# Optimization experiments

Measured on AMD Instinct MI355X. Metric: run time of the kernel, lower is better.

Reference implementation:

```python
import jax, jax.numpy as jnp
import numpy as np

B, N, DIM = 32, 1024, 512
H, KD, ATTN_RATIO = 8, 64, 4
D = ATTN_RATIO * KD            # value dim per head = 256
DH = D * H                     # 2048
QKV_OUT = DH + 2 * H * KD      # 3072
RES = 32                       # resolution (32, 32), N = 32*32
SCALE = KD ** -0.5


def _make_bias_idxs(res):
    coords = np.stack(np.meshgrid(np.arange(res), np.arange(res), indexing="ij"), -1).reshape(-1, 2)  # [N,2]
    off = np.abs(coords[:, None, :] - coords[None, :, :])  # [N,N,2]
    return jnp.asarray(off[..., 0] * res + off[..., 1], dtype=jnp.int32)  # [N,N] in [0, res*res)


def setup_inputs() -> dict:
    key = jax.random.key(0)
    ks = jax.random.split(key, 6)
    x = jax.random.normal(ks[0], (B, N, DIM), dtype=jnp.float32)
    gamma = jnp.ones((DIM,), jnp.float32)
    beta = jnp.zeros((DIM,), jnp.float32)
    qkv_w = jax.random.normal(ks[1], (DIM, QKV_OUT), jnp.float32) * 0.02
    qkv_b = jnp.zeros((QKV_OUT,), jnp.float32)
    proj_w = jax.random.normal(ks[2], (DH, DIM), jnp.float32) * 0.02
    proj_b = jnp.zeros((DIM,), jnp.float32)
    biases = jax.random.normal(ks[3], (H, RES * RES), jnp.float32) * 0.02
    bias_idxs = _make_bias_idxs(RES)
    return {"x": x, "gamma": gamma, "beta": beta, "qkv_w": qkv_w, "qkv_b": qkv_b,
            "proj_w": proj_w, "proj_b": proj_b, "biases": biases, "bias_idxs": bias_idxs}


def reference(x, gamma, beta, qkv_w, qkv_b, proj_w, proj_b, biases, bias_idxs):
    # LayerNorm
    mu = jnp.mean(x, axis=-1, keepdims=True)
    var = jnp.mean(jnp.square(x - mu), axis=-1, keepdims=True)
    xn = (x - mu) * jax.lax.rsqrt(var + 1e-5) * gamma + beta
    # QKV projection and head split
    qkv = (xn @ qkv_w + qkv_b).reshape(B, N, H, 2 * KD + D)
    q, k, v = jnp.split(qkv, [KD, 2 * KD], axis=-1)  # [B,N,H,KD],[B,N,H,KD],[B,N,H,D]
    # Attention with relative-position bias
    bias = biases[:, bias_idxs]  # [H,N,N]
    attn = jnp.einsum("bqhd,bkhd->bhqk", q, k) * SCALE + bias[None]
    attn = jax.nn.softmax(attn, axis=-1)
    out = jnp.einsum("bhqk,bkhd->bqhd", attn, v).reshape(B, N, DH)
    return out @ proj_w + proj_b
```

## Files before the change

### kernel.cpp

```cpp
#include <hip/hip_runtime.h>
#include <hip/hip_bf16.h>
#include <initializer_list>

typedef _Float16 half8 __attribute__((ext_vector_type(8)));
typedef float floatx4 __attribute__((ext_vector_type(4)));

#define MFMA16(a, b, c) __builtin_amdgcn_mfma_f32_16x16x32_f16((a), (b), (c), 0, 0, 0)

__device__ __forceinline__ void gload16(const void* g, void* l) {
    __builtin_amdgcn_global_load_lds((const __attribute__((address_space(1))) unsigned int*)g,
                                     (__attribute__((address_space(3))) unsigned int*)l,
                                     16, 0, 0);
}

__global__ __launch_bounds__(256) void ln_kernel(const float* __restrict__ x,
                                                 const float* __restrict__ gamma,
                                                 const float* __restrict__ beta,
                                                 _Float16* __restrict__ xn) {
    int row = blockIdx.x;
    int tid = threadIdx.x;
    float2 v = ((const float2*)(x + (size_t)row * 512))[tid];

    __shared__ float red[4];
    __shared__ float mv[2];

    float s = v.x + v.y;
#pragma unroll
    for (int o = 32; o > 0; o >>= 1) s += __shfl_down(s, o);
    if ((tid & 63) == 0) red[tid >> 6] = s;
    __syncthreads();
    if (tid == 0) mv[0] = (red[0] + red[1] + red[2] + red[3]) * (1.f / 512.f);
    __syncthreads();
    float mean = mv[0];

    float dx = v.x - mean, dy = v.y - mean;
    float sq = dx * dx + dy * dy;
#pragma unroll
    for (int o = 32; o > 0; o >>= 1) sq += __shfl_xor(sq, o);
    __syncthreads();
    if ((tid & 63) == 0) red[tid >> 6] = sq;
    __syncthreads();
    if (tid == 0) mv[1] = rsqrtf((red[0] + red[1] + red[2] + red[3]) * (1.f / 512.f) + 1e-5f);
    __syncthreads();
    float rstd = mv[1];

    float g0 = gamma[tid * 2], g1 = gamma[tid * 2 + 1];
    float b0 = beta[tid * 2], b1 = beta[tid * 2 + 1];
    union { _Float16 h[2]; unsigned int u; } pk;
    pk.h[0] = (_Float16)(dx * rstd * g0 + b0);
    pk.h[1] = (_Float16)(dy * rstd * g1 + b1);
    ((unsigned int*)(xn + (size_t)row * 512))[tid] = pk.u;
}

__global__ __launch_bounds__(256) void transpose_cast(const float* __restrict__ in,
                                                      _Float16* __restrict__ out,
                                                      int R, int C) {
    __shared__ float t[32][33];
    int c0 = blockIdx.x * 32, r0 = blockIdx.y * 32;
    int tx = threadIdx.x & 31, ty = threadIdx.x >> 5;
#pragma unroll
    for (int j = 0; j < 4; ++j)
        t[ty + j * 8][tx] = in[(size_t)(r0 + ty + j * 8) * C + c0 + tx];
    __syncthreads();
#pragma unroll
    for (int j = 0; j < 4; ++j)
        out[(size_t)(c0 + ty + j * 8) * R + r0 + tx] = (_Float16)t[tx][ty + j * 8];
}

template <int OUTMODE>
__global__ __launch_bounds__(256) void gemm_bt(const _Float16* __restrict__ A,
                                               const _Float16* __restrict__ Bt,
                                               const float* __restrict__ bias,
                                               void* __restrict__ Cout,
                                               _Float16* __restrict__ Vt,
                                               int M, int N, int K) {
    __shared__ __align__(16) _Float16 Asb[128 * 32];
    __shared__ __align__(16) _Float16 Bsb[128 * 32];

    int m0 = blockIdx.x * 128;
    int n0 = blockIdx.y * 128;
    int tid = threadIdx.x;
    int w = tid >> 6, lane = tid & 63, lrow = lane & 15, quad = lane >> 4;
    int wm = (w >> 1) * 64, wn = (w & 1) * 64;

    int hh = 0, part = 0;
    bool sw = false;
    if (OUTMODE == 2) {
        hh = blockIdx.y / 3;
        part = blockIdx.y - hh * 3;
        sw = (part != 0);
    }

    int srow = lane >> 2;
    int scb = (lane & 3) ^ ((lane >> 3) & 3);
    const _Float16* Abase = A + (size_t)(m0 + w * 16 + srow) * K + scb * 8;
    const _Float16* Bbase = Bt + (size_t)(n0 + w * 16 + srow) * K + scb * 8;
    char* AldsB = (char*)Asb + w * 1024;
    char* BldsB = (char*)Bsb + w * 1024;
    const size_t rowskip = (size_t)64 * K;

    int swz = (lrow >> 1) & 3;

    floatx4 acc[4][4];
#pragma unroll
    for (int i = 0; i < 4; ++i)
#pragma unroll
        for (int j = 0; j < 4; ++j) acc[i][j] = (floatx4){0.f, 0.f, 0.f, 0.f};

    for (int k0 = 0; k0 < K; k0 += 32) {
        __syncthreads();
        gload16(Abase + k0, AldsB);
        gload16(Abase + rowskip + k0, AldsB + 4096);
        gload16(Bbase + k0, BldsB);
        gload16(Bbase + rowskip + k0, BldsB + 4096);
        __syncthreads();

        half8 af[4], bf[4];
#pragma unroll
        for (int i = 0; i < 4; ++i) {
            int r = wm + i * 16 + lrow;
            af[i] = *(const half8*)&Asb[r * 32 + (quad ^ swz) * 8];
        }
#pragma unroll
        for (int j = 0; j < 4; ++j) {
            int r = wn + j * 16 + lrow;
            bf[j] = *(const half8*)&Bsb[r * 32 + (quad ^ swz) * 8];
        }
        if (OUTMODE == 2 && sw) {
#pragma unroll
            for (int i = 0; i < 4; ++i)
#pragma unroll
                for (int j = 0; j < 4; ++j)
                    acc[i][j] = MFMA16(bf[j], af[i], acc[i][j]);
        } else {
#pragma unroll
            for (int i = 0; i < 4; ++i)
#pragma unroll
                for (int j = 0; j < 4; ++j)
                    acc[i][j] = MFMA16(af[i], bf[j], acc[i][j]);
        }
    }

    if (OUTMODE == 2 && sw) {
        int b_rel = m0 >> 10;
        int tok0 = (m0 & 1023) + wm;
        _Float16* vbase = Vt + (((size_t)b_rel * 8 + hh) * 256 + (part - 1) * 128) * 1024;
#pragma unroll
        for (int j = 0; j < 4; ++j)
#pragma unroll
            for (int r = 0; r < 4; ++r) {
                int d = wn + j * 16 + quad * 4 + r;
                float bv = bias[n0 + d];
                _Float16* vrow = vbase + (size_t)d * 1024 + tok0;
#pragma unroll
                for (int i = 0; i < 4; ++i)
                    vrow[i * 16 + lrow] = (_Float16)(acc[i][j][r] + bv);
            }
        return;
    }

#pragma unroll
    for (int i = 0; i < 4; ++i)
#pragma unroll
        for (int j = 0; j < 4; ++j) {
            int colg = n0 + wn + j * 16 + lrow;
            int coll = wn + j * 16 + lrow;
            float bv = bias[colg];
#pragma unroll
            for (int r = 0; r < 4; ++r) {
                int rowg = m0 + wm + i * 16 + quad * 4 + r;
                float v = acc[i][j][r] + bv;
                if (OUTMODE == 1) {
                    ((float*)Cout)[(size_t)rowg * N + colg] = v;
                } else {
                    ((_Float16*)Cout)[(size_t)rowg * 1024 + hh * 128 + coll] = (_Float16)v;
                }
            }
        }
}

__global__ __launch_bounds__(256) void attn_kernel(const _Float16* __restrict__ qk,
                                                   const _Float16* __restrict__ vt,
                                                   const float* __restrict__ biases,
                                                   _Float16* __restrict__ out) {
    int h  = blockIdx.x & 7;
    int qt = (blockIdx.x >> 3) | (blockIdx.y << 1);
    int b  = blockIdx.z;

    int tid = threadIdx.x;
    int w = tid >> 6, lane = tid & 63, lrow = lane & 15, quad = lane >> 4;

    __shared__ float bias_lds[1024];
    __shared__ __align__(16) _Float16 K_lds[32 * 72];
    __shared__ __align__(16) _Float16 V_t[256 * 32];

    for (int i = tid; i < 1024; i += 256) bias_lds[i] = biases[h * 1024 + i];

    int qrow = qt * 64 + w * 16 + lrow;
    const _Float16* qbase = qk + ((size_t)(b * 1024 + qrow)) * 1024 + h * 128;
    half8 aq0 = *(const half8*)(qbase + quad * 8);
    half8 aq1 = *(const half8*)(qbase + 32 + quad * 8);

    int key_l = tid >> 3, kd8 = (tid & 7) * 8;
    const _Float16* ksrc = qk + ((size_t)(b * 1024 + key_l)) * 1024 + h * 128 + 64 + kd8;
    int cc = tid & 3;
    const _Float16* vsrc0 = vt + ((size_t)((b * 8 + h) * 256 + (tid >> 2))) * 1024 + cc * 4;

    int qr = qrow >> 5, qc = qrow & 31;
    int bcol0[4], bcol1[4];
#pragma unroll
    for (int r = 0; r < 4; ++r) {
        bcol0[r] = abs(qc - (quad * 4 + r));
        bcol1[r] = abs(qc - (16 + quad * 4 + r));
    }

    float m_r = -1e30f, l_r = 0.f;
    floatx4 od[16];
#pragma unroll
    for (int dt = 0; dt < 16; ++dt) od[dt] = (floatx4){0.f, 0.f, 0.f, 0.f};

    uint4 kreg;
    uint2 vA[4], vB[4];

    kreg = *(const uint4*)ksrc;
#pragma unroll
    for (int it = 0; it < 4; ++it) {
        const _Float16* p = vsrc0 + (size_t)it * 64 * 1024;
        vA[it] = *(const uint2*)p;
        vB[it] = *(const uint2*)(p + 16);
    }

    for (int kt = 0; kt < 32; ++kt) {
        *(uint4*)&K_lds[key_l * 72 + kd8] = kreg;
#pragma unroll
        for (int it = 0; it < 4; ++it) {
            uint4 v;
            v.x = vA[it].x; v.y = vA[it].y; v.z = vB[it].x; v.w = vB[it].y;
            *(uint4*)&V_t[((tid >> 2) + it * 64) * 32 + cc * 8] = v;
        }
        __syncthreads();

        if (kt < 31) {
            kreg = *(const uint4*)(ksrc + (size_t)(kt + 1) * 32 * 1024);
            const _Float16* vp = vsrc0 + (size_t)(kt + 1) * 32;
#pragma unroll
            for (int it = 0; it < 4; ++it) {
                const _Float16* p = vp + (size_t)it * 64 * 1024;
                vA[it] = *(const uint2*)p;
                vB[it] = *(const uint2*)(p + 16);
            }
        }

        floatx4 sc0 = (floatx4){0.f, 0.f, 0.f, 0.f}, sc1 = sc0;
        {
            half8 kf;
            kf = *(const half8*)&K_lds[lrow * 72 + quad * 8];              sc0 = MFMA16(kf, aq0, sc0);
            kf = *(const half8*)&K_lds[lrow * 72 + 32 + quad * 8];         sc0 = MFMA16(kf, aq1, sc0);
            kf = *(const half8*)&K_lds[(16 + lrow) * 72 + quad * 8];       sc1 = MFMA16(kf, aq0, sc1);
            kf = *(const half8*)&K_lds[(16 + lrow) * 72 + 32 + quad * 8];  sc1 = MFMA16(kf, aq1, sc1);
        }

        int rowoff = abs(qr - kt) << 5;
        float s0[4], s1[4];
#pragma unroll
        for (int r = 0; r < 4; ++r) {
            s0[r] = sc0[r] * 0.125f + bias_lds[rowoff + bcol0[r]];
            s1[r] = sc1[r] * 0.125f + bias_lds[rowoff + bcol1[r]];
        }

        float pmax = fmaxf(fmaxf(fmaxf(s0[0], s0[1]), fmaxf(s0[2], s0[3])),
                           fmaxf(fmaxf(s1[0], s1[1]), fmaxf(s1[2], s1[3])));
        pmax = fmaxf(pmax, __shfl_xor(pmax, 16));
        pmax = fmaxf(pmax, __shfl_xor(pmax, 32));

        if (!__all(pmax - m_r <= 8.f)) {
            float mnew = fmaxf(m_r, pmax);
            float alpha = __expf(m_r - mnew);
            m_r = mnew;
            l_r *= alpha;
            float a4[4];
#pragma unroll
            for (int r = 0; r < 4; ++r) a4[r] = __shfl(alpha, quad * 4 + r, 16);
#pragma unroll
            for (int dt = 0; dt < 16; ++dt)
#pragma unroll
                for (int r = 0; r < 4; ++r) od[dt][r] *= a4[r];
        }

        float p0[4], p1[4], rs = 0.f;
#pragma unroll
        for (int r = 0; r < 4; ++r) { p0[r] = __expf(s0[r] - m_r); rs += p0[r]; }
#pragma unroll
        for (int r = 0; r < 4; ++r) { p1[r] = __expf(s1[r] - m_r); rs += p1[r]; }
        rs += __shfl_xor(rs, 16);
        rs += __shfl_xor(rs, 32);
        l_r += rs;

        union H8 { _Float16 h[8]; half8 v; } pa;
#pragma unroll
        for (int r = 0; r < 4; ++r) { pa.h[r] = (_Float16)p0[r]; pa.h[4 + r] = (_Float16)p1[r]; }

#pragma unroll
        for (int dt = 0; dt < 16; ++dt) {
            half8 bv = *(const half8*)&V_t[(dt * 16 + lrow) * 32 + quad * 8];
            od[dt] = MFMA16(pa.v, bv, od[dt]);
        }
        __syncthreads();
    }

#pragma unroll
    for (int r = 0; r < 4; ++r) {
        float lq = __shfl(l_r, quad * 4 + r, 16);
        float inv = 1.f / lq;
        int qg = qt * 64 + w * 16 + quad * 4 + r;
        _Float16* orow = out + ((size_t)(b * 1024 + qg)) * 2048 + h * 256;
#pragma unroll
        for (int dt = 0; dt < 16; ++dt)
            orow[dt * 16 + lrow] = (_Float16)(od[dt][r] * inv);
    }
}

extern "C" void kernel_launch(void* const* d_in, const int* in_sizes, int n_in,
                              void* d_out, int out_size, void* d_ws, size_t ws_size,
                              hipStream_t stream) {
    const float* x      = (const float*)d_in[0];
    const float* gamma  = (const float*)d_in[1];
    const float* beta   = (const float*)d_in[2];
    const float* qkv_w  = (const float*)d_in[3];
    const float* qkv_b  = (const float*)d_in[4];
    const float* proj_w = (const float*)d_in[5];
    const float* proj_b = (const float*)d_in[6];
    const float* biases = (const float*)d_in[7];

    float* out = (float*)d_out;

    _Float16* ws      = (_Float16*)d_ws;
    _Float16* qkv_wt  = ws;
    _Float16* proj_wt = qkv_wt + (size_t)512 * 3072;
    _Float16* xn      = proj_wt + (size_t)2048 * 512;
    _Float16* chunk0  = xn + (size_t)32768 * 512;

    const size_t FIXED_HALVES = (size_t)512 * 3072 + (size_t)2048 * 512 + (size_t)32768 * 512;
    int CB = 0;
    for (int cb : {16, 8, 4, 2, 1}) {
        size_t halves = FIXED_HALVES + (size_t)cb * 1024 * (1024 + 2048 + 2048);
        if (halves * sizeof(_Float16) <= ws_size) { CB = cb; break; }
    }
    if (CB == 0) return;
    _Float16* qk_c  = chunk0;
    _Float16* vt_c  = qk_c + (size_t)CB * 1024 * 1024;
    _Float16* att_c = vt_c + (size_t)CB * 1024 * 2048;

    transpose_cast<<<dim3(3072 / 32, 512 / 32), 256, 0, stream>>>(qkv_w, qkv_wt, 512, 3072);
    transpose_cast<<<dim3(512 / 32, 2048 / 32), 256, 0, stream>>>(proj_w, proj_wt, 2048, 512);
    ln_kernel<<<32768, 256, 0, stream>>>(x, gamma, beta, xn);

    const int MC = CB * 1024;
    for (int c = 0; c < 32 / CB; ++c) {
        const _Float16* xn_c = xn + (size_t)c * MC * 512;
        gemm_bt<2><<<dim3(MC / 128, 24), 256, 0, stream>>>(xn_c, qkv_wt, qkv_b,
                                                           (void*)qk_c, vt_c, MC, 3072, 512);
        attn_kernel<<<dim3(16, 8, CB), 256, 0, stream>>>(qk_c, vt_c, biases, att_c);
        float* out_c = out + (size_t)c * MC * 512;
        gemm_bt<1><<<dim3(MC / 128, 4), 256, 0, stream>>>(att_c, proj_wt, proj_b,
                                                          (void*)out_c, nullptr, MC, 512, 2048);
    }
}
```

Baseline: 791.6 us.

## Double query rows per wave and double-buffer K/V tiles in attention

```diff
diff --git a/kernel.cpp b/kernel.cpp
--- a/kernel.cpp
+++ b/kernel.cpp
@@ -183,141 +183,166 @@
                                                    const _Float16* __restrict__ vt,
                                                    const float* __restrict__ biases,
                                                    _Float16* __restrict__ out) {
-    int h  = blockIdx.x & 7;
-    int qt = (blockIdx.x >> 3) | (blockIdx.y << 1);
+    int h  = blockIdx.x;
+    int qt = blockIdx.y;
     int b  = blockIdx.z;
 
     int tid = threadIdx.x;
     int w = tid >> 6, lane = tid & 63, lrow = lane & 15, quad = lane >> 4;
 
     __shared__ float bias_lds[1024];
-    __shared__ __align__(16) _Float16 K_lds[32 * 72];
-    __shared__ __align__(16) _Float16 V_t[256 * 32];
+    __shared__ __align__(16) _Float16 K_lds[2][32 * 72];
+    __shared__ __align__(16) _Float16 V_s[2][256 * 32];
 
     for (int i = tid; i < 1024; i += 256) bias_lds[i] = biases[h * 1024 + i];
 
-    int qrow = qt * 64 + w * 16 + lrow;
-    const _Float16* qbase = qk + ((size_t)(b * 1024 + qrow)) * 1024 + h * 128;
-    half8 aq0 = *(const half8*)(qbase + quad * 8);
-    half8 aq1 = *(const half8*)(qbase + 32 + quad * 8);
+    int q0 = qt * 128 + w * 32 + lrow;
+    const _Float16* qb = qk + ((size_t)(b * 1024 + q0)) * 1024 + h * 128;
+    half8 aq[2][2];
+    aq[0][0] = *(const half8*)(qb + quad * 8);
+    aq[0][1] = *(const half8*)(qb + 32 + quad * 8);
+    aq[1][0] = *(const half8*)(qb + 16 * 1024 + quad * 8);
+    aq[1][1] = *(const half8*)(qb + 16 * 1024 + 32 + quad * 8);
 
     int key_l = tid >> 3, kd8 = (tid & 7) * 8;
     const _Float16* ksrc = qk + ((size_t)(b * 1024 + key_l)) * 1024 + h * 128 + 64 + kd8;
     int cc = tid & 3;
     const _Float16* vsrc0 = vt + ((size_t)((b * 8 + h) * 256 + (tid >> 2))) * 1024 + cc * 4;
 
-    int qr = qrow >> 5, qc = qrow & 31;
-    int bcol0[4], bcol1[4];
-#pragma unroll
-    for (int r = 0; r < 4; ++r) {
-        bcol0[r] = abs(qc - (quad * 4 + r));
-        bcol1[r] = abs(qc - (16 + quad * 4 + r));
-    }
-
-    float m_r = -1e30f, l_r = 0.f;
-    floatx4 od[16];
-#pragma unroll
-    for (int dt = 0; dt < 16; ++dt) od[dt] = (floatx4){0.f, 0.f, 0.f, 0.f};
+    int qr = qt * 4 + w;
+
+    float m_[2] = {-1e30f, -1e30f}, l_[2] = {0.f, 0.f};
+    floatx4 od[2][16];
+#pragma unroll
+    for (int f = 0; f < 2; ++f)
+#pragma unroll
+        for (int dt = 0; dt < 16; ++dt) od[f][dt] = (floatx4){0.f, 0.f, 0.f, 0.f};
 
     uint4 kreg;
     uint2 vA[4], vB[4];
 
-    kreg = *(const uint4*)ksrc;
-#pragma unroll
-    for (int it = 0; it < 4; ++it) {
-        const _Float16* p = vsrc0 + (size_t)it * 64 * 1024;
-        vA[it] = *(const uint2*)p;
-        vB[it] = *(const uint2*)(p + 16);
-    }
+#define LOADT(t)                                                          \
+    do {                                                                  \
+        kreg = *(const uint4*)(ksrc + (size_t)(t) * 32 * 1024);           \
+        const _Float16* vp = vsrc0 + (size_t)(t) * 32;                    \
+        _Pragma("unroll") for (int it = 0; it < 4; ++it) {                \
+            const _Float16* p = vp + (size_t)it * 64 * 1024;              \
+            vA[it] = *(const uint2*)p;                                    \
+            vB[it] = *(const uint2*)(p + 16);                             \
+        }                                                                 \
+    } while (0)
+
+#define WRITET(bb)                                                        \
+    do {                                                                  \
+        *(uint4*)&K_lds[bb][key_l * 72 + kd8] = kreg;                     \
+        _Pragma("unroll") for (int it = 0; it < 4; ++it) {                \
+            uint4 v;                                                      \
+            v.x = vA[it].x; v.y = vA[it].y; v.z = vB[it].x; v.w = vB[it].y; \
+            *(uint4*)&V_s[bb][((tid >> 2) + it * 64) * 32 + cc * 8] = v;  \
+        }                                                                 \
+    } while (0)
+
+    LOADT(0);
+    WRITET(0);
+    LOADT(1);
+    __syncthreads();
 
     for (int kt = 0; kt < 32; ++kt) {
-        *(uint4*)&K_lds[key_l * 72 + kd8] = kreg;
-#pragma unroll
-        for (int it = 0; it < 4; ++it) {
-            uint4 v;
-            v.x = vA[it].x; v.y = vA[it].y; v.z = vB[it].x; v.w = vB[it].y;
-            *(uint4*)&V_t[((tid >> 2) + it * 64) * 32 + cc * 8] = v;
+        int bufc = kt & 1;
+        const _Float16* Kc = K_lds[bufc];
+        const _Float16* Vc = V_s[bufc];
+
+        floatx4 sc[2][2];
+#pragma unroll
+        for (int f = 0; f < 2; ++f)
+#pragma unroll
+            for (int t = 0; t < 2; ++t) sc[f][t] = (floatx4){0.f, 0.f, 0.f, 0.f};
+        {
+            half8 kf00 = *(const half8*)&Kc[lrow * 72 + quad * 8];
+            half8 kf01 = *(const half8*)&Kc[lrow * 72 + 32 + quad * 8];
+            half8 kf10 = *(const half8*)&Kc[(16 + lrow) * 72 + quad * 8];
+            half8 kf11 = *(const half8*)&Kc[(16 + lrow) * 72 + 32 + quad * 8];
+#pragma unroll
+            for (int f = 0; f < 2; ++f) {
+                sc[f][0] = MFMA16(kf00, aq[f][0], sc[f][0]);
+                sc[f][0] = MFMA16(kf01, aq[f][1], sc[f][0]);
+                sc[f][1] = MFMA16(kf10, aq[f][0], sc[f][1]);
+                sc[f][1] = MFMA16(kf11, aq[f][1], sc[f][1]);
+            }
+        }
+
+        int rowoff = abs(qr - kt) << 5;
+        union H8 { _Float16 hh[8]; half8 v; } pa[2];
+
+#pragma unroll
+        for (int f = 0; f < 2; ++f) {
+            int qcf = lrow + f * 16;
+            float s_[8];
+#pragma unroll
+            for (int t = 0; t < 2; ++t)
+#pragma unroll
+                for (int r = 0; r < 4; ++r) {
+                    int kc = t * 16 + quad * 4 + r;
+                    s_[t * 4 + r] = sc[f][t][r] * 0.125f + bias_lds[rowoff + abs(qcf - kc)];
+                }
+
+            float pmax = fmaxf(fmaxf(fmaxf(s_[0], s_[1]), fmaxf(s_[2], s_[3])),
+                               fmaxf(fmaxf(s_[4], s_[5]), fmaxf(s_[6], s_[7])));
+            pmax = fmaxf(pmax, __shfl_xor(pmax, 16));
+            pmax = fmaxf(pmax, __shfl_xor(pmax, 32));
+
+            if (!__all(pmax - m_[f] <= 8.f)) {
+                float mnew = fmaxf(m_[f], pmax);
+                float alpha = __expf(m_[f] - mnew);
+                m_[f] = mnew;
+                l_[f] *= alpha;
+                float a4[4];
+#pragma unroll
+                for (int r = 0; r < 4; ++r) a4[r] = __shfl(alpha, quad * 4 + r, 16);
+#pragma unroll
+                for (int dt = 0; dt < 16; ++dt)
+#pragma unroll
+                    for (int r = 0; r < 4; ++r) od[f][dt][r] *= a4[r];
+            }
+
+            float rs = 0.f;
+#pragma unroll
+            for (int i = 0; i < 8; ++i) {
+                float p = __expf(s_[i] - m_[f]);
+                pa[f].hh[i] = (_Float16)p;
+                rs += p;
+            }
+            rs += __shfl_xor(rs, 16);
+            rs += __shfl_xor(rs, 32);
+            l_[f] += rs;
+        }
+
+        if (kt < 31) WRITET(bufc ^ 1);
+        if (kt < 30) LOADT(kt + 2);
+
+#pragma unroll
+        for (int dt = 0; dt < 16; ++dt) {
+            half8 bv = *(const half8*)&Vc[(dt * 16 + lrow) * 32 + quad * 8];
+            od[0][dt] = MFMA16(pa[0].v, bv, od[0][dt]);
+            od[1][dt] = MFMA16(pa[1].v, bv, od[1][dt]);
         }
         __syncthreads();
-
-        if (kt < 31) {
-            kreg = *(const uint4*)(ksrc + (size_t)(kt + 1) * 32 * 1024);
-            const _Float16* vp = vsrc0 + (size_t)(kt + 1) * 32;
-#pragma unroll
-            for (int it = 0; it < 4; ++it) {
-                const _Float16* p = vp + (size_t)it * 64 * 1024;
-                vA[it] = *(const uint2*)p;
-                vB[it] = *(const uint2*)(p + 16);
-            }
-        }
-
-        floatx4 sc0 = (floatx4){0.f, 0.f, 0.f, 0.f}, sc1 = sc0;
-        {
-            half8 kf;
-            kf = *(const half8*)&K_lds[lrow * 72 + quad * 8];              sc0 = MFMA16(kf, aq0, sc0);
-            kf = *(const half8*)&K_lds[lrow * 72 + 32 + quad * 8];         sc0 = MFMA16(kf, aq1, sc0);
-            kf = *(const half8*)&K_lds[(16 + lrow) * 72 + quad * 8];       sc1 = MFMA16(kf, aq0, sc1);
-            kf = *(const half8*)&K_lds[(16 + lrow) * 72 + 32 + quad * 8];  sc1 = MFMA16(kf, aq1, sc1);
-        }
-
-        int rowoff = abs(qr - kt) << 5;
-        float s0[4], s1[4];
+    }
+#undef LOADT
+#undef WRITET
+
+#pragma unroll
+    for (int f = 0; f < 2; ++f)
 #pragma unroll
         for (int r = 0; r < 4; ++r) {
-            s0[r] = sc0[r] * 0.125f + bias_lds[rowoff + bcol0[r]];
-            s1[r] = sc1[r] * 0.125f + bias_lds[rowoff + bcol1[r]];
-        }
-
-        float pmax = fmaxf(fmaxf(fmaxf(s0[0], s0[1]), fmaxf(s0[2], s0[3])),
-                           fmaxf(fmaxf(s1[0], s1[1]), fmaxf(s1[2], s1[3])));
-        pmax = fmaxf(pmax, __shfl_xor(pmax, 16));
-        pmax = fmaxf(pmax, __shfl_xor(pmax, 32));
-
-        if (!__all(pmax - m_r <= 8.f)) {
-            float mnew = fmaxf(m_r, pmax);
-            float alpha = __expf(m_r - mnew);
-            m_r = mnew;
-            l_r *= alpha;
-            float a4[4];
-#pragma unroll
-            for (int r = 0; r < 4; ++r) a4[r] = __shfl(alpha, quad * 4 + r, 16);
+            float lq = __shfl(l_[f], quad * 4 + r, 16);
+            float inv = 1.f / lq;
+            int qg = qt * 128 + w * 32 + f * 16 + quad * 4 + r;
+            _Float16* orow = out + ((size_t)(b * 1024 + qg)) * 2048 + h * 256;
 #pragma unroll
             for (int dt = 0; dt < 16; ++dt)
-#pragma unroll
-                for (int r = 0; r < 4; ++r) od[dt][r] *= a4[r];
-        }
-
-        float p0[4], p1[4], rs = 0.f;
-#pragma unroll
-        for (int r = 0; r < 4; ++r) { p0[r] = __expf(s0[r] - m_r); rs += p0[r]; }
-#pragma unroll
-        for (int r = 0; r < 4; ++r) { p1[r] = __expf(s1[r] - m_r); rs += p1[r]; }
-        rs += __shfl_xor(rs, 16);
-        rs += __shfl_xor(rs, 32);
-        l_r += rs;
-
-        union H8 { _Float16 h[8]; half8 v; } pa;
-#pragma unroll
-        for (int r = 0; r < 4; ++r) { pa.h[r] = (_Float16)p0[r]; pa.h[4 + r] = (_Float16)p1[r]; }
-
-#pragma unroll
-        for (int dt = 0; dt < 16; ++dt) {
-            half8 bv = *(const half8*)&V_t[(dt * 16 + lrow) * 32 + quad * 8];
-            od[dt] = MFMA16(pa.v, bv, od[dt]);
-        }
-        __syncthreads();
-    }
-
-#pragma unroll
-    for (int r = 0; r < 4; ++r) {
-        float lq = __shfl(l_r, quad * 4 + r, 16);
-        float inv = 1.f / lq;
-        int qg = qt * 64 + w * 16 + quad * 4 + r;
-        _Float16* orow = out + ((size_t)(b * 1024 + qg)) * 2048 + h * 256;
-#pragma unroll
-        for (int dt = 0; dt < 16; ++dt)
-            orow[dt * 16 + lrow] = (_Float16)(od[dt][r] * inv);
-    }
+                orow[dt * 16 + lrow] = (_Float16)(od[f][dt][r] * inv);
+        }
 }
 
 extern "C" void kernel_launch(void* const* d_in, const int* in_sizes, int n_in,
@@ -360,7 +385,7 @@
         const _Float16* xn_c = xn + (size_t)c * MC * 512;
         gemm_bt<2><<<dim3(MC / 128, 24), 256, 0, stream>>>(xn_c, qkv_wt, qkv_b,
                                                            (void*)qk_c, vt_c, MC, 3072, 512);
-        attn_kernel<<<dim3(16, 8, CB), 256, 0, stream>>>(qk_c, vt_c, biases, att_c);
+        attn_kernel<<<dim3(8, 8, CB), 256, 0, stream>>>(qk_c, vt_c, biases, att_c);
         float* out_c = out + (size_t)c * MC * 512;
         gemm_bt<1><<<dim3(MC / 128, 4), 256, 0, stream>>>(att_c, proj_wt, proj_b,
                                                           (void*)out_c, nullptr, MC, 512, 2048);
```

After: 836.3 us. +5.7%, slower.
